# Kernel tuning notes

Measured on AMD Instinct MI355X. Metric: run time of the kernel, lower is better.

The kernel has to match this reference:

```python
import jax, jax.numpy as jnp
import numpy as np

N_DRUG, N_GENE = 20000, 40000
D_DRUG, D_GENE = 128, 64
HID, EMB = 64, 32
E_DD, E_DG, E_GG = 1500000, 1000000, 1500000


def setup_inputs() -> dict:
    key = jax.random.key(0)
    ks = iter(jax.random.split(key, 32))

    def nrm(shape, scale=0.05):
        return jax.random.normal(next(ks), shape, dtype=jnp.float32) * scale

    def idx(n, e):
        return jax.random.randint(next(ks), (e,), 0, n, dtype=jnp.int32)

    return dict(
        feat_drug=nrm((N_DRUG, D_DRUG), 1.0),
        feat_gene=nrm((N_GENE, D_GENE), 1.0),
        dd_src=idx(N_DRUG, E_DD), dd_dst=idx(N_DRUG, E_DD),
        dg_src=idx(N_DRUG, E_DG), dg_dst=idx(N_GENE, E_DG),
        gg_src=idx(N_GENE, E_GG), gg_dst=idx(N_GENE, E_GG),
        neg_src=idx(N_DRUG, E_DD), neg_dst=idx(N_DRUG, E_DD),
        W1_dd=nrm((D_DRUG, HID)), W1_dg=nrm((D_DRUG, HID)), W1_gg=nrm((D_GENE, HID)),
        W1_self_drug=nrm((D_DRUG, HID)), W1_self_gene=nrm((D_GENE, HID)),
        b1=jnp.zeros((HID,), jnp.float32),
        W2_dd=nrm((HID, EMB)), W2_dg=nrm((HID, EMB)), W2_gg=nrm((HID, EMB)),
        W2_self_drug=nrm((HID, EMB)), W2_self_gene=nrm((HID, EMB)),
        b2=jnp.zeros((EMB,), jnp.float32),
        w_rel=nrm((EMB,), 1.0),
    )


def _mean_agg(msg_nodes, src, dst, n_dst):
    # transform-then-gather: msg_nodes is [n_src, out]; gather per edge, scatter-sum to dst,
    # divide by dst in-degree (DGL GraphConv norm='right').
    m = jax.ops.segment_sum(msg_nodes[src], dst, num_segments=n_dst)
    deg = jax.ops.segment_sum(jnp.ones(dst.shape, msg_nodes.dtype), dst, num_segments=n_dst)
    return m / jnp.clip(deg, 1.0)[:, None]


def _rel_layer(hd, hg, edges, Wdd, Wdg, Wgg, Wsd, Wsg, b, act):
    dd_src, dd_dst, dg_src, dg_dst, gg_src, gg_dst = edges
    # per-relation linear transform on src nodes, then mean aggregation to dst;
    # sum across relations sharing the same dst node type (HeteroGraphConv aggregate='sum')
    agg_d = _mean_agg(hd @ Wdd, dd_src, dd_dst, hd.shape[0])
    agg_g = (_mean_agg(hd @ Wdg, dg_src, dg_dst, hg.shape[0])
             + _mean_agg(hg @ Wgg, gg_src, gg_dst, hg.shape[0]))
    out_d = agg_d + hd @ Wsd + b  # self-loop + bias
    out_g = agg_g + hg @ Wsg + b
    if act:
        out_d, out_g = jax.nn.relu(out_d), jax.nn.relu(out_g)
    return out_d, out_g


def reference(feat_drug, feat_gene, dd_src, dd_dst, dg_src, dg_dst, gg_src, gg_dst,
              neg_src, neg_dst, W1_dd, W1_dg, W1_gg, W1_self_drug, W1_self_gene, b1,
              W2_dd, W2_dg, W2_gg, W2_self_drug, W2_self_gene, b2, w_rel):
    edges = (dd_src, dd_dst, dg_src, dg_dst, gg_src, gg_dst)
    h_d, h_g = _rel_layer(feat_drug, feat_gene, edges,
                          W1_dd, W1_dg, W1_gg, W1_self_drug, W1_self_gene, b1, True)
    h_d, h_g = _rel_layer(h_d, h_g, edges,
                          W2_dd, W2_dg, W2_gg, W2_self_drug, W2_self_gene, b2, False)
    # per-edge-type diagonal-bilinear dot-product scorer, etype='dd' (drug-drug)
    pos = jnp.sum(h_d[dd_src] * w_rel * h_d[dd_dst], axis=-1)
    neg = jnp.sum(h_d[neg_src] * w_rel * h_d[neg_dst], axis=-1)
    return pos, neg
```

## Files before the change

### kernel.cpp

```cpp
#include <hip/hip_runtime.h>


template<int KIN, int KOUT>
__global__ __launch_bounds__(256) void gemm_kernel(const float* __restrict__ A,
                                                   const float* __restrict__ W,
                                                   float* __restrict__ out, int M) {
    __shared__ float Ws[KIN * KOUT];
    const int tid = threadIdx.y * KOUT + threadIdx.x;
    for (int i = tid; i < KIN * KOUT; i += 256) Ws[i] = W[i];
    __syncthreads();
    const int n = threadIdx.x;
    const int ROWS = 256 / KOUT;
    for (int m = blockIdx.x * ROWS + threadIdx.y; m < M; m += gridDim.x * ROWS) {
        const float* a = A + (size_t)m * KIN;
        float acc = 0.0f;
#pragma unroll
        for (int k = 0; k < KIN; ++k) acc = fmaf(a[k], Ws[k * KOUT + n], acc);
        out[(size_t)m * KOUT + n] = acc;
    }
}

__global__ __launch_bounds__(256) void degree_int_kernel(const int* __restrict__ dst,
                                                         int* __restrict__ deg, int E) {
    for (int e = blockIdx.x * blockDim.x + threadIdx.x; e < E;
         e += gridDim.x * blockDim.x)
        atomicAdd(&deg[dst[e]], 1);
}

__global__ __launch_bounds__(1024) void scan_kernel(const int* __restrict__ deg,
                                                    int* __restrict__ off, int N) {
    __shared__ int part[1024];
    const int t = threadIdx.x;
    const int per = (N + 1023) / 1024;
    const int beg = t * per;
    const int end = min(beg + per, N);
    int s = 0;
    for (int i = beg; i < end; ++i) s += deg[i];
    part[t] = s;
    __syncthreads();
    for (int d = 1; d < 1024; d <<= 1) {
        int v = (t >= d) ? part[t - d] : 0;
        __syncthreads();
        part[t] += v;
        __syncthreads();
    }
    int run = (t == 0) ? 0 : part[t - 1];
    for (int i = beg; i < end; ++i) { off[i] = run; run += deg[i]; }
    if (t == 1023) off[N] = part[1023];
}

__global__ __launch_bounds__(256) void fill_kernel(const int* __restrict__ src,
                                                   const int* __restrict__ dst,
                                                   const int* __restrict__ off,
                                                   int* __restrict__ cursor,
                                                   int* __restrict__ csr_src, int E) {
    for (int e = blockIdx.x * blockDim.x + threadIdx.x; e < E;
         e += gridDim.x * blockDim.x) {
        const int d = dst[e];
        const int p = off[d] + atomicAdd(&cursor[d], 1);
        csr_src[p] = src[e];
    }
}

template<int W, bool RELU>
__global__ __launch_bounds__(256) void gather_combine_kernel(
        const float* __restrict__ msg, const int* __restrict__ csr_src,
        const int* __restrict__ off, const float* __restrict__ selfb,
        const float* __restrict__ b, float* __restrict__ out, int N) {
    const int GRP = 256 / W;
    const int g = threadIdx.x / W;
    const int lane = threadIdx.x % W;
    const float bk = b[lane];
    for (int n = blockIdx.x * GRP + g; n < N; n += gridDim.x * GRP) {
        const int beg = off[n], end = off[n + 1];
        float acc = 0.0f;
        int i = beg;
        for (; i + 4 <= end; i += 4) {
            const int s0 = csr_src[i], s1 = csr_src[i + 1];
            const int s2 = csr_src[i + 2], s3 = csr_src[i + 3];
            const float v0 = msg[(size_t)s0 * W + lane];
            const float v1 = msg[(size_t)s1 * W + lane];
            const float v2 = msg[(size_t)s2 * W + lane];
            const float v3 = msg[(size_t)s3 * W + lane];
            acc += (v0 + v1) + (v2 + v3);
        }
        for (; i < end; ++i) acc += msg[(size_t)csr_src[i] * W + lane];
        const float d = (end > beg) ? (float)(end - beg) : 1.0f;
        float v = acc / d + selfb[(size_t)n * W + lane] + bk;
        if (RELU) v = fmaxf(v, 0.0f);
        out[(size_t)n * W + lane] = v;
    }
}

__global__ __launch_bounds__(256) void score_kernel(const float* __restrict__ h,
                                                    const int* __restrict__ src,
                                                    const int* __restrict__ dst,
                                                    const float* __restrict__ wrel,
                                                    float* __restrict__ out, int E) {
    const int lj = threadIdx.x & 7;
    const size_t gid = (size_t)blockIdx.x * blockDim.x + threadIdx.x;
    const size_t grp = gid >> 3;
    const size_t ngrp = ((size_t)gridDim.x * blockDim.x) >> 3;
    const float4 w = *(const float4*)(wrel + lj * 4);
    for (size_t e = grp; e < (size_t)E; e += ngrp) {
        const int s = src[e], d = dst[e];
        const float4 hs = *(const float4*)(h + (size_t)s * 32 + lj * 4);
        const float4 hd = *(const float4*)(h + (size_t)d * 32 + lj * 4);
        float p = hs.x * w.x * hd.x + hs.y * w.y * hd.y +
                  hs.z * w.z * hd.z + hs.w * w.w * hd.w;
        p += __shfl_xor(p, 1, 64);
        p += __shfl_xor(p, 2, 64);
        p += __shfl_xor(p, 4, 64);
        if (lj == 0) out[e] = p;
    }
}

static inline int grid_for(size_t n, int cap) {
    size_t b = (n + 255) / 256;
    if (b > (size_t)cap) b = (size_t)cap;
    if (b < 1) b = 1;
    return (int)b;
}

extern "C" void kernel_launch(void* const* d_in, const int* in_sizes, int n_in,
                              void* d_out, int out_size, void* d_ws, size_t ws_size,
                              hipStream_t stream) {
    const float* feat_drug    = (const float*)d_in[0];
    const int*   dd_src       = (const int*)d_in[2];
    const int*   dd_dst       = (const int*)d_in[3];
    const int*   neg_src      = (const int*)d_in[8];
    const int*   neg_dst      = (const int*)d_in[9];
    const float* W1_dd        = (const float*)d_in[10];
    const float* W1_self_drug = (const float*)d_in[13];
    const float* b1           = (const float*)d_in[15];
    const float* W2_dd        = (const float*)d_in[16];
    const float* W2_self_drug = (const float*)d_in[19];
    const float* b2           = (const float*)d_in[21];
    const float* w_rel        = (const float*)d_in[22];

    const int N  = in_sizes[0] / 128;
    const int E  = in_sizes[2];
    const int EN = in_sizes[8];

    char* ws = (char*)d_ws;
    int*   deg_i   = (int*)ws;                         ws += (size_t)N * 4;
    int*   cursor  = (int*)ws;                         ws += (size_t)N * 4;
    int*   off     = (int*)ws;                         ws += (size_t)(N + 1) * 4;
    int*   csr_src = (int*)ws;                         ws += (size_t)E * 4;
    float* msg1    = (float*)ws;                       ws += (size_t)N * 64 * 4;
    float* self1   = (float*)ws;                       ws += (size_t)N * 64 * 4;
    float* h1      = (float*)ws;                       ws += (size_t)N * 64 * 4;
    float* msg2    = (float*)ws;                       ws += (size_t)N * 32 * 4;
    float* self2   = (float*)ws;                       ws += (size_t)N * 32 * 4;
    float* h2      = (float*)ws;                       ws += (size_t)N * 32 * 4;

    float* pos = (float*)d_out;
    float* neg = pos + E;

    hipMemsetAsync(deg_i,  0, (size_t)N * sizeof(int), stream);
    hipMemsetAsync(cursor, 0, (size_t)N * sizeof(int), stream);

    degree_int_kernel<<<grid_for(E, 2048), 256, 0, stream>>>(dd_dst, deg_i, E);
    scan_kernel<<<1, 1024, 0, stream>>>(deg_i, off, N);
    fill_kernel<<<grid_for(E, 2048), 256, 0, stream>>>(dd_src, dd_dst, off, cursor, csr_src, E);

    gemm_kernel<128, 64><<<(N + 3) / 4, dim3(64, 4), 0, stream>>>(feat_drug, W1_dd, msg1, N);
    gemm_kernel<128, 64><<<(N + 3) / 4, dim3(64, 4), 0, stream>>>(feat_drug, W1_self_drug, self1, N);
    gather_combine_kernel<64, true><<<(N + 3) / 4, 256, 0, stream>>>(msg1, csr_src, off, self1, b1, h1, N);

    gemm_kernel<64, 32><<<(N + 7) / 8, dim3(32, 8), 0, stream>>>(h1, W2_dd, msg2, N);
    gemm_kernel<64, 32><<<(N + 7) / 8, dim3(32, 8), 0, stream>>>(h1, W2_self_drug, self2, N);
    gather_combine_kernel<32, false><<<(N + 7) / 8, 256, 0, stream>>>(msg2, csr_src, off, self2, b2, h2, N);

    score_kernel<<<grid_for((size_t)E * 8, 4096), 256, 0, stream>>>(h2, dd_src, dd_dst, w_rel, pos, E);
    score_kernel<<<grid_for((size_t)EN * 8, 4096), 256, 0, stream>>>(h2, neg_src, neg_dst, w_rel, neg, EN);
}
```

Before: 396.3 us.

## Partition CSR build by destination range and fuse paired GEMMs and score launches

Degree counting and CSR fill now run with blocks split into 8 destination-range partitions. Each block scans all edges but only applies atomics for its own range, so atomic traffic stays in a smaller address window and gets better cache locality. The fill cursor is seeded with the offsets during the scan, which removes a memset and an offset lookup. The gather then uses the final cursor as each segment's end. The message and self-loop GEMMs are fused into one kernel per layer so the input is read once, and the positive and negative score kernels are merged into one launch. The cost is that every partition reads the full edge arrays, 8x redundant index traffic.

```diff
diff --git a/kernel.cpp b/kernel.cpp
--- a/kernel.cpp
+++ b/kernel.cpp
@@ -1,34 +1,52 @@
 #include <hip/hip_runtime.h>
 
 
+#define NPART 8
+
 template<int KIN, int KOUT>
-__global__ __launch_bounds__(256) void gemm_kernel(const float* __restrict__ A,
-                                                   const float* __restrict__ W,
-                                                   float* __restrict__ out, int M) {
-    __shared__ float Ws[KIN * KOUT];
+__global__ __launch_bounds__(256) void gemm2_kernel(const float* __restrict__ A,
+                                                    const float* __restrict__ Wa,
+                                                    const float* __restrict__ Wb,
+                                                    float* __restrict__ out_a,
+                                                    float* __restrict__ out_b, int M) {
+    __shared__ float Wsa[KIN * KOUT];
+    __shared__ float Wsb[KIN * KOUT];
     const int tid = threadIdx.y * KOUT + threadIdx.x;
-    for (int i = tid; i < KIN * KOUT; i += 256) Ws[i] = W[i];
+    for (int i = tid; i < KIN * KOUT; i += 256) { Wsa[i] = Wa[i]; Wsb[i] = Wb[i]; }
     __syncthreads();
     const int n = threadIdx.x;
     const int ROWS = 256 / KOUT;
     for (int m = blockIdx.x * ROWS + threadIdx.y; m < M; m += gridDim.x * ROWS) {
         const float* a = A + (size_t)m * KIN;
-        float acc = 0.0f;
+        float aa = 0.0f, ab = 0.0f;
 #pragma unroll
-        for (int k = 0; k < KIN; ++k) acc = fmaf(a[k], Ws[k * KOUT + n], acc);
-        out[(size_t)m * KOUT + n] = acc;
-    }
-}
-
-__global__ __launch_bounds__(256) void degree_int_kernel(const int* __restrict__ dst,
-                                                         int* __restrict__ deg, int E) {
-    for (int e = blockIdx.x * blockDim.x + threadIdx.x; e < E;
-         e += gridDim.x * blockDim.x)
-        atomicAdd(&deg[dst[e]], 1);
+        for (int k = 0; k < KIN; ++k) {
+            const float av = a[k];
+            aa = fmaf(av, Wsa[k * KOUT + n], aa);
+            ab = fmaf(av, Wsb[k * KOUT + n], ab);
+        }
+        out_a[(size_t)m * KOUT + n] = aa;
+        out_b[(size_t)m * KOUT + n] = ab;
+    }
+}
+
+__global__ __launch_bounds__(256) void degree_part_kernel(const int* __restrict__ dst,
+                                                          int* __restrict__ deg,
+                                                          int E, int psz) {
+    const int part = blockIdx.x & (NPART - 1);
+    const int lo = part * psz, hi = lo + psz;
+    const int bpp = gridDim.x >> 3;
+    const int bip = blockIdx.x >> 3;
+    const int stride = bpp * 256;
+    for (int e = bip * 256 + threadIdx.x; e < E; e += stride) {
+        const int d = dst[e];
+        if (d >= lo && d < hi) atomicAdd(&deg[d], 1);
+    }
 }
 
 __global__ __launch_bounds__(1024) void scan_kernel(const int* __restrict__ deg,
-                                                    int* __restrict__ off, int N) {
+                                                    int* __restrict__ off,
+                                                    int* __restrict__ cursor, int N) {
     __shared__ int part[1024];
     const int t = threadIdx.x;
     const int per = (N + 1023) / 1024;
@@ -45,34 +63,42 @@
         __syncthreads();
     }
     int run = (t == 0) ? 0 : part[t - 1];
-    for (int i = beg; i < end; ++i) { off[i] = run; run += deg[i]; }
+    for (int i = beg; i < end; ++i) { off[i] = run; cursor[i] = run; run += deg[i]; }
     if (t == 1023) off[N] = part[1023];
 }
 
-__global__ __launch_bounds__(256) void fill_kernel(const int* __restrict__ src,
-                                                   const int* __restrict__ dst,
-                                                   const int* __restrict__ off,
-                                                   int* __restrict__ cursor,
-                                                   int* __restrict__ csr_src, int E) {
-    for (int e = blockIdx.x * blockDim.x + threadIdx.x; e < E;
-         e += gridDim.x * blockDim.x) {
+__global__ __launch_bounds__(256) void fill_part_kernel(const int* __restrict__ src,
+                                                        const int* __restrict__ dst,
+                                                        int* __restrict__ cursor,
+                                                        int* __restrict__ csr_src,
+                                                        int E, int psz) {
+    const int part = blockIdx.x & (NPART - 1);
+    const int lo = part * psz, hi = lo + psz;
+    const int bpp = gridDim.x >> 3;
+    const int bip = blockIdx.x >> 3;
+    const int stride = bpp * 256;
+    for (int e = bip * 256 + threadIdx.x; e < E; e += stride) {
         const int d = dst[e];
-        const int p = off[d] + atomicAdd(&cursor[d], 1);
-        csr_src[p] = src[e];
+        const int s = src[e];
+        if (d >= lo && d < hi) {
+            const int p = atomicAdd(&cursor[d], 1);
+            csr_src[p] = s;
+        }
     }
 }
 
 template<int W, bool RELU>
 __global__ __launch_bounds__(256) void gather_combine_kernel(
         const float* __restrict__ msg, const int* __restrict__ csr_src,
-        const int* __restrict__ off, const float* __restrict__ selfb,
-        const float* __restrict__ b, float* __restrict__ out, int N) {
+        const int* __restrict__ off, const int* __restrict__ endp,
+        const float* __restrict__ selfb, const float* __restrict__ b,
+        float* __restrict__ out, int N) {
     const int GRP = 256 / W;
     const int g = threadIdx.x / W;
     const int lane = threadIdx.x % W;
     const float bk = b[lane];
     for (int n = blockIdx.x * GRP + g; n < N; n += gridDim.x * GRP) {
-        const int beg = off[n], end = off[n + 1];
+        const int beg = off[n], end = endp[n];
         float acc = 0.0f;
         int i = beg;
         for (; i + 4 <= end; i += 4) {
@@ -92,18 +118,24 @@
     }
 }
 
-__global__ __launch_bounds__(256) void score_kernel(const float* __restrict__ h,
-                                                    const int* __restrict__ src,
-                                                    const int* __restrict__ dst,
-                                                    const float* __restrict__ wrel,
-                                                    float* __restrict__ out, int E) {
+__global__ __launch_bounds__(256) void score2_kernel(const float* __restrict__ h,
+                                                     const int* __restrict__ sA,
+                                                     const int* __restrict__ dA,
+                                                     const int* __restrict__ sB,
+                                                     const int* __restrict__ dB,
+                                                     const float* __restrict__ wrel,
+                                                     float* __restrict__ outA,
+                                                     float* __restrict__ outB,
+                                                     int EA, int EB) {
     const int lj = threadIdx.x & 7;
-    const size_t gid = (size_t)blockIdx.x * blockDim.x + threadIdx.x;
-    const size_t grp = gid >> 3;
+    const size_t grp = ((size_t)blockIdx.x * blockDim.x + threadIdx.x) >> 3;
     const size_t ngrp = ((size_t)gridDim.x * blockDim.x) >> 3;
     const float4 w = *(const float4*)(wrel + lj * 4);
-    for (size_t e = grp; e < (size_t)E; e += ngrp) {
-        const int s = src[e], d = dst[e];
+    const size_t total = (size_t)EA + (size_t)EB;
+    for (size_t e = grp; e < total; e += ngrp) {
+        int s, d; float* o;
+        if (e < (size_t)EA) { s = sA[e]; d = dA[e]; o = outA + e; }
+        else { const size_t e2 = e - EA; s = sB[e2]; d = dB[e2]; o = outB + e2; }
         const float4 hs = *(const float4*)(h + (size_t)s * 32 + lj * 4);
         const float4 hd = *(const float4*)(h + (size_t)d * 32 + lj * 4);
         float p = hs.x * w.x * hd.x + hs.y * w.y * hd.y +
@@ -111,15 +143,8 @@
         p += __shfl_xor(p, 1, 64);
         p += __shfl_xor(p, 2, 64);
         p += __shfl_xor(p, 4, 64);
-        if (lj == 0) out[e] = p;
-    }
-}
-
-static inline int grid_for(size_t n, int cap) {
-    size_t b = (n + 255) / 256;
-    if (b > (size_t)cap) b = (size_t)cap;
-    if (b < 1) b = 1;
-    return (int)b;
+        if (lj == 0) *o = p;
+    }
 }
 
 extern "C" void kernel_launch(void* const* d_in, const int* in_sizes, int n_in,
@@ -141,11 +166,12 @@
     const int N  = in_sizes[0] / 128;
     const int E  = in_sizes[2];
     const int EN = in_sizes[8];
+    const int PSZ = (N + NPART - 1) / NPART;
 
     char* ws = (char*)d_ws;
     int*   deg_i   = (int*)ws;                         ws += (size_t)N * 4;
-    int*   cursor  = (int*)ws;                         ws += (size_t)N * 4;
     int*   off     = (int*)ws;                         ws += (size_t)(N + 1) * 4;
+    int*   cursor  = (int*)ws;                         ws += (size_t)(N + 1) * 4;
     int*   csr_src = (int*)ws;                         ws += (size_t)E * 4;
     float* msg1    = (float*)ws;                       ws += (size_t)N * 64 * 4;
     float* self1   = (float*)ws;                       ws += (size_t)N * 64 * 4;
@@ -157,21 +183,22 @@
     float* pos = (float*)d_out;
     float* neg = pos + E;
 
-    hipMemsetAsync(deg_i,  0, (size_t)N * sizeof(int), stream);
-    hipMemsetAsync(cursor, 0, (size_t)N * sizeof(int), stream);
-
-    degree_int_kernel<<<grid_for(E, 2048), 256, 0, stream>>>(dd_dst, deg_i, E);
-    scan_kernel<<<1, 1024, 0, stream>>>(deg_i, off, N);
-    fill_kernel<<<grid_for(E, 2048), 256, 0, stream>>>(dd_src, dd_dst, off, cursor, csr_src, E);
-
-    gemm_kernel<128, 64><<<(N + 3) / 4, dim3(64, 4), 0, stream>>>(feat_drug, W1_dd, msg1, N);
-    gemm_kernel<128, 64><<<(N + 3) / 4, dim3(64, 4), 0, stream>>>(feat_drug, W1_self_drug, self1, N);
-    gather_combine_kernel<64, true><<<(N + 3) / 4, 256, 0, stream>>>(msg1, csr_src, off, self1, b1, h1, N);
-
-    gemm_kernel<64, 32><<<(N + 7) / 8, dim3(32, 8), 0, stream>>>(h1, W2_dd, msg2, N);
-    gemm_kernel<64, 32><<<(N + 7) / 8, dim3(32, 8), 0, stream>>>(h1, W2_self_drug, self2, N);
-    gather_combine_kernel<32, false><<<(N + 7) / 8, 256, 0, stream>>>(msg2, csr_src, off, self2, b2, h2, N);
-
-    score_kernel<<<grid_for((size_t)E * 8, 4096), 256, 0, stream>>>(h2, dd_src, dd_dst, w_rel, pos, E);
-    score_kernel<<<grid_for((size_t)EN * 8, 4096), 256, 0, stream>>>(h2, neg_src, neg_dst, w_rel, neg, EN);
-}
+    hipMemsetAsync(deg_i, 0, (size_t)N * sizeof(int), stream);
+
+    degree_part_kernel<<<512, 256, 0, stream>>>(dd_dst, deg_i, E, PSZ);
+    scan_kernel<<<1, 1024, 0, stream>>>(deg_i, off, cursor, N);
+    fill_part_kernel<<<512, 256, 0, stream>>>(dd_src, dd_dst, cursor, csr_src, E, PSZ);
+
+    gemm2_kernel<128, 64><<<(N + 3) / 4, dim3(64, 4), 0, stream>>>(
+        feat_drug, W1_dd, W1_self_drug, msg1, self1, N);
+    gather_combine_kernel<64, true><<<(N + 3) / 4, 256, 0, stream>>>(
+        msg1, csr_src, off, cursor, self1, b1, h1, N);
+
+    gemm2_kernel<64, 32><<<(N + 7) / 8, dim3(32, 8), 0, stream>>>(
+        h1, W2_dd, W2_self_drug, msg2, self2, N);
+    gather_combine_kernel<32, false><<<(N + 7) / 8, 256, 0, stream>>>(
+        msg2, csr_src, off, cursor, self2, b2, h2, N);
+
+    score2_kernel<<<4096, 256, 0, stream>>>(h2, dd_src, dd_dst, neg_src, neg_dst,
+                                            w_rel, pos, neg, E, EN);
+}
```

New measurement: 459.9 us. +16.1%, slower.
